# Kernel optimization log

Measured on AMD Instinct MI355X. Metric: run time of the kernel, lower is better.

The kernel has to match this reference:

```python
import jax, jax.numpy as jnp
import numpy as np

RADIUS = 0.4
NSAMPLE = 32
NORMALIZE_DP = True


def setup_inputs() -> dict:
    key = jax.random.key(0)
    k1, k2, k3 = jax.random.split(key, 3)
    B, N, K, C = 2, 16384, 4096, 128
    xyz = jax.random.normal(k1, (B, N, 3), dtype=jnp.float32)
    new_xyz = jax.random.normal(k2, (B, K, 3), dtype=jnp.float32)
    features = jax.random.normal(k3, (B, C, N), dtype=jnp.float32)
    return {"xyz": xyz, "new_xyz": new_xyz, "features": features}


def _ball_query(radius, nsample, xyz, new_xyz):
    # xyz: (B,N,3), new_xyz: (B,K,3) -> indices (B,K,nsample) int32
    N = xyz.shape[1]
    # squared distances via ||a||^2 + ||b||^2 - 2 a.b  -> (B,K,N)
    d2 = (jnp.sum(new_xyz * new_xyz, -1)[:, :, None]
          + jnp.sum(xyz * xyz, -1)[:, None, :]
          - 2.0 * jnp.einsum('bkd,bnd->bkn', new_xyz, xyz))
    mask = d2 < radius * radius
    # key = point index if inside ball else N (sentinel); take nsample smallest
    key = jnp.where(mask, jnp.arange(N, dtype=jnp.int32), jnp.int32(N))
    neg_top, _ = jax.lax.top_k(-key, nsample)  # (B,K,nsample)
    idx = -neg_top
    # pointnet2 semantics: pad with first in-radius index (0 if ball empty)
    first = idx[..., :1]
    first = jnp.where(first < N, first, 0)
    idx = jnp.where(idx < N, idx, first)
    return idx


def _group(features, idx):
    # features: (B,C,N), idx: (B,K,ns) -> (B,C,K,ns)
    return jax.vmap(lambda f, i: f[:, i])(features, idx)


def reference(xyz, new_xyz, features):
    idx = _ball_query(RADIUS, NSAMPLE, xyz, new_xyz)          # (B,K,ns)
    xyz_t = jnp.transpose(xyz, (0, 2, 1))                      # (B,3,N)
    grouped_xyz = _group(xyz_t, idx)                           # (B,3,K,ns)
    grouped_xyz = grouped_xyz - jnp.transpose(new_xyz, (0, 2, 1))[..., None]
    if NORMALIZE_DP:
        grouped_xyz = grouped_xyz / RADIUS
    grouped_features = _group(features, idx)                   # (B,C,K,ns)
    return (grouped_xyz, grouped_features)
```

## Files before the change

kernel.cpp:

```cpp
#include <hip/hip_runtime.h>

#define BB 2
#define NN 16384
#define KK 4096
#define CC 128
#define SS 32

typedef float vfloat4 __attribute__((ext_vector_type(4)));

__global__ __launch_bounds__(256) void transpose_prep_kernel(
    const float* __restrict__ feat, const float* __restrict__ xyz,
    float* __restrict__ feat_t, float* __restrict__ xyzw)
{
    __shared__ float tile[64][133];
    const int b  = blockIdx.x >> 8;
    const int n0 = (blockIdx.x & 255) * 64;
    const int t  = threadIdx.x;

    if (t < 64) {
        const int i = b * NN + n0 + t;
        const float* p = xyz + (size_t)i * 3;
        const float x = p[0], y = p[1], z = p[2];
        const float pp = __fadd_rn(__fadd_rn(__fmul_rn(x, x), __fmul_rn(y, y)),
                                   __fmul_rn(z, z));
        vfloat4 v = {x, y, z, pp};
        *(vfloat4*)(xyzw + (size_t)i * 4) = v;
    }

    const int ln = t & 63;
    const int cr = t >> 6;
#pragma unroll
    for (int p = 0; p < 32; ++p) {
        const int c = p * 4 + cr;
        tile[ln][c] = feat[((size_t)b * CC + c) * NN + n0 + ln];
    }
    __syncthreads();

    const int cl = t & 31;
    const int ns = t >> 5;
#pragma unroll
    for (int p = 0; p < 8; ++p) {
        const int n = ns + 8 * p;
        float* dst = feat_t + ((size_t)(b * NN + n0 + n)) * CC;
#pragma unroll
        for (int j = 0; j < 4; ++j)
            dst[cl + 32 * j] = tile[n][cl + 32 * j];
    }
}

__global__ __launch_bounds__(256) void ball_query_kernel(
    const float* __restrict__ xyzw,
    const float* __restrict__ new_xyz,
    int* __restrict__ idx_buf)
{
    __shared__ vfloat4 pts[256];

    const int t    = threadIdx.x;
    const int wave = t >> 6;
    const int lane = t & 63;
    const int qi   = blockIdx.x * 4 + wave;
    const int b    = qi >> 12;
    const int k    = qi & (KK - 1);

    const float R2 = (float)(0.4 * 0.4);

    const float* q = new_xyz + (size_t)(b * KK + k) * 3;
    const float qx = q[0], qy = q[1], qz = q[2];
    const float qq = __fadd_rn(__fadd_rn(__fmul_rn(qx, qx), __fmul_rn(qy, qy)),
                               __fmul_rn(qz, qz));

    const vfloat4* xw = (const vfloat4*)xyzw + (size_t)b * NN;
    int* out = idx_buf + (size_t)qi * SS;

    int cnt = 0;

    pts[t] = xw[t];
    __syncthreads();

    for (int base = 0; base < NN; base += 256) {
        const int nb = (base + 256 < NN) ? base + 256 : 0;
        const vfloat4 nxt = xw[nb + t];

        if (cnt < SS) {
            vfloat4 v0 = pts[lane];
            vfloat4 v1 = pts[64 + lane];
            vfloat4 v2 = pts[128 + lane];
            vfloat4 v3 = pts[192 + lane];

            auto d2test = [&](vfloat4 v) -> bool {
                const float dot = __fadd_rn(
                    __fadd_rn(__fmul_rn(qx, v.x), __fmul_rn(qy, v.y)),
                    __fmul_rn(qz, v.z));
                const float d2 = __fsub_rn(__fadd_rn(qq, v.w), __fmul_rn(2.0f, dot));
                return d2 < R2;
            };

            const bool i0 = d2test(v0);
            const bool i1 = d2test(v1);
            const bool i2 = d2test(v2);
            const bool i3 = d2test(v3);
            const unsigned long long m0 = __ballot(i0);
            const unsigned long long m1 = __ballot(i1);
            const unsigned long long m2 = __ballot(i2);
            const unsigned long long m3 = __ballot(i3);

            const int c0 = cnt;
            const int p0 = __popcll(m0), p1 = __popcll(m1);
            const int p2 = __popcll(m2), p3 = __popcll(m3);
            cnt = c0 + p0 + p1 + p2 + p3;

            if ((m0 | m1 | m2 | m3) != 0ull && c0 < SS) {
                const unsigned long long lt = (1ull << lane) - 1ull;
                int bs = c0;
                if (i0) { const int pos = bs + __popcll(m0 & lt);
                          if (pos < SS) out[pos] = base + lane; }
                bs += p0;
                if (i1) { const int pos = bs + __popcll(m1 & lt);
                          if (pos < SS) out[pos] = base + 64 + lane; }
                bs += p1;
                if (i2) { const int pos = bs + __popcll(m2 & lt);
                          if (pos < SS) out[pos] = base + 128 + lane; }
                bs += p2;
                if (i3) { const int pos = bs + __popcll(m3 & lt);
                          if (pos < SS) out[pos] = base + 192 + lane; }
            }
        }

        if (__syncthreads_and(cnt >= SS)) break;

        pts[t] = nxt;
        __syncthreads();
    }

    const int fill = (cnt > 0) ? out[0] : 0;
    if (lane < SS && lane >= cnt) out[lane] = fill;
}

__global__ __launch_bounds__(256) void group_kernel(
    const float* __restrict__ xyzw,
    const float* __restrict__ new_xyz,
    const float* __restrict__ feat_t,
    const int*   __restrict__ idx_buf,
    float* __restrict__ out)
{
    __shared__ float tile[SS * CC];
    __shared__ float txyz[3][SS];

    const int t    = threadIdx.x;
    const int l    = t & 63;
    const int w    = t >> 6;
    const int bk   = blockIdx.x;
    const int b    = bk >> 12;
    const int k    = bk & (KK - 1);
    const int half = l >> 5;
    const int cl   = l & 31;

#pragma unroll
    for (int p = 0; p < 4; ++p) {
        const int r = 8 * w + 2 * p;
        const int s = r + half;
        const int n = idx_buf[bk * SS + s];
        const int chunk = cl ^ ((s >> 2) & 7);
        const float* src = feat_t + ((size_t)(b * NN + n)) * CC + 4 * chunk;
        __builtin_amdgcn_global_load_lds(
            (const __attribute__((address_space(1))) void*)src,
            (__attribute__((address_space(3))) void*)(tile + r * CC),
            16, 0, 0);
    }

    if (t < SS) {
        const int n = idx_buf[bk * SS + t];
        const float* q = new_xyz + (size_t)bk * 3;
        const vfloat4 wv = *((const vfloat4*)xyzw + (size_t)b * NN + n);
        txyz[0][t] = (wv.x - q[0]) / 0.4f;
        txyz[1][t] = (wv.y - q[1]) / 0.4f;
        txyz[2][t] = (wv.z - q[2]) / 0.4f;
    }

    __syncthreads();

    float* out_xyz  = out;
    float* out_feat = out + (size_t)BB * 3 * KK * SS;

    const int sq = t & 7;
    const int c0 = t >> 3;
#pragma unroll
    for (int p = 0; p < 4; ++p) {
        const int c  = c0 + 32 * p;
        const int co = (((c >> 2) ^ sq) << 2) + (c & 3);
        vfloat4 v;
        v.x = tile[(4 * sq + 0) * CC + co];
        v.y = tile[(4 * sq + 1) * CC + co];
        v.z = tile[(4 * sq + 2) * CC + co];
        v.w = tile[(4 * sq + 3) * CC + co];
        __builtin_nontemporal_store(
            v, (vfloat4*)(out_feat + (((size_t)(b * CC + c) * KK + k) * SS + 4 * sq)));
    }

    if (t < 24) {
        const int d   = t >> 3;
        const int sq2 = t & 7;
        const vfloat4 v = *(vfloat4*)&txyz[d][4 * sq2];
        __builtin_nontemporal_store(
            v, (vfloat4*)(out_xyz + (((size_t)(b * 3 + d) * KK + k) * SS + 4 * sq2)));
    }
}

extern "C" void kernel_launch(void* const* d_in, const int* in_sizes, int n_in,
                              void* d_out, int out_size, void* d_ws, size_t ws_size,
                              hipStream_t stream) {
    const float* xyz     = (const float*)d_in[0];
    const float* new_xyz = (const float*)d_in[1];
    const float* feat    = (const float*)d_in[2];
    float* out = (float*)d_out;

    int*   idx_buf = (int*)d_ws;
    float* xyzw    = (float*)((char*)d_ws + (1 << 20));
    float* feat_t  = (float*)((char*)d_ws + (1 << 20) + (512 << 10));

    transpose_prep_kernel<<<dim3(BB * (NN / 64)), dim3(256), 0, stream>>>(
        feat, xyz, feat_t, xyzw);

    ball_query_kernel<<<dim3(BB * KK / 4), dim3(256), 0, stream>>>(
        xyzw, new_xyz, idx_buf);

    group_kernel<<<dim3(BB * KK), dim3(256), 0, stream>>>(
        xyzw, new_xyz, feat_t, idx_buf, out);
}
```

Measured before the change: 101.6 us.

## Sort queries by radial distance to balance ball-query early exit; vectorize transpose

Adds a single-block kernel that buckets query points by squared norm (per batch) and writes a permutation, so that each ball-query block handles four queries with similar distance from the origin and therefore similar early-exit points. This is meant to cut the time waves spend waiting on the slowest query in a block, and to order blocks by cost. The feature transpose now uses float4 global loads and stores instead of scalar ones. The costs are an extra serial single-block launch, scattered LDS atomics, and a qmap indirection.

```diff
diff --git a/kernel.cpp b/kernel.cpp
--- a/kernel.cpp
+++ b/kernel.cpp
@@ -5,6 +5,7 @@
 #define KK 4096
 #define CC 128
 #define SS 32
+#define BKK (BB * KK)
 
 typedef float vfloat4 __attribute__((ext_vector_type(4)));
 
@@ -27,30 +28,78 @@
         *(vfloat4*)(xyzw + (size_t)i * 4) = v;
     }
 
-    const int ln = t & 63;
-    const int cr = t >> 6;
-#pragma unroll
-    for (int p = 0; p < 32; ++p) {
-        const int c = p * 4 + cr;
-        tile[ln][c] = feat[((size_t)b * CC + c) * NN + n0 + ln];
-    }
-    __syncthreads();
-
-    const int cl = t & 31;
-    const int ns = t >> 5;
-#pragma unroll
-    for (int p = 0; p < 8; ++p) {
-        const int n = ns + 8 * p;
-        float* dst = feat_t + ((size_t)(b * NN + n0 + n)) * CC;
-#pragma unroll
-        for (int j = 0; j < 4; ++j)
-            dst[cl + 32 * j] = tile[n][cl + 32 * j];
+#pragma unroll
+    for (int i = 0; i < 8; ++i) {
+        const int li = i * 256 + t;
+        const int c  = li >> 4;
+        const int n4 = (li & 15) * 4;
+        const vfloat4 v = *(const vfloat4*)(feat + ((size_t)b * CC + c) * NN + n0 + n4);
+        tile[n4 + 0][c] = v.x;
+        tile[n4 + 1][c] = v.y;
+        tile[n4 + 2][c] = v.z;
+        tile[n4 + 3][c] = v.w;
+    }
+    __syncthreads();
+
+#pragma unroll
+    for (int i = 0; i < 8; ++i) {
+        const int li = i * 256 + t;
+        const int n  = li >> 5;
+        const int c4 = (li & 31) * 4;
+        vfloat4 v;
+        v.x = tile[n][c4 + 0];
+        v.y = tile[n][c4 + 1];
+        v.z = tile[n][c4 + 2];
+        v.w = tile[n][c4 + 3];
+        *(vfloat4*)(feat_t + ((size_t)(b * NN + n0 + n)) * CC + c4) = v;
+    }
+}
+
+__global__ __launch_bounds__(1024) void qsort_kernel(
+    const float* __restrict__ new_xyz,
+    int* __restrict__ qmap)
+{
+    __shared__ int hist[128];
+    __shared__ int base[128];
+    __shared__ unsigned char bk[BKK];
+
+    const int t = threadIdx.x;
+    if (t < 128) hist[t] = 0;
+    __syncthreads();
+
+#pragma unroll
+    for (int c = 0; c < BKK / 1024; ++c) {
+        const int q = c * 1024 + t;
+        const int b = q >> 12;
+        const float* p = new_xyz + (size_t)q * 3;
+        const float qq = p[0] * p[0] + p[1] * p[1] + p[2] * p[2];
+        int bkt = (int)(qq * 8.0f);
+        bkt = bkt > 63 ? 63 : bkt;
+        bkt |= (b << 6);
+        bk[q] = (unsigned char)bkt;
+        atomicAdd(&hist[bkt], 1);
+    }
+    __syncthreads();
+
+    if (t == 0) {
+        int s = 0;
+#pragma unroll
+        for (int i = 0; i < 128; ++i) { base[i] = s; s += hist[i]; }
+    }
+    __syncthreads();
+
+#pragma unroll
+    for (int c = 0; c < BKK / 1024; ++c) {
+        const int q = c * 1024 + t;
+        const int pos = atomicAdd(&base[bk[q]], 1);
+        qmap[pos] = q;
     }
 }
 
 __global__ __launch_bounds__(256) void ball_query_kernel(
     const float* __restrict__ xyzw,
     const float* __restrict__ new_xyz,
+    const int* __restrict__ qmap,
     int* __restrict__ idx_buf)
 {
     __shared__ vfloat4 pts[256];
@@ -58,7 +107,7 @@
     const int t    = threadIdx.x;
     const int wave = t >> 6;
     const int lane = t & 63;
-    const int qi   = blockIdx.x * 4 + wave;
+    const int qi   = qmap[blockIdx.x * 4 + wave];
     const int b    = qi >> 12;
     const int k    = qi & (KK - 1);
 
@@ -217,13 +266,16 @@
     int*   idx_buf = (int*)d_ws;
     float* xyzw    = (float*)((char*)d_ws + (1 << 20));
     float* feat_t  = (float*)((char*)d_ws + (1 << 20) + (512 << 10));
+    int*   qmap    = (int*)((char*)d_ws + (1 << 20) + (512 << 10) + (CC * NN * BB) * 4);
 
     transpose_prep_kernel<<<dim3(BB * (NN / 64)), dim3(256), 0, stream>>>(
         feat, xyz, feat_t, xyzw);
 
-    ball_query_kernel<<<dim3(BB * KK / 4), dim3(256), 0, stream>>>(
-        xyzw, new_xyz, idx_buf);
-
-    group_kernel<<<dim3(BB * KK), dim3(256), 0, stream>>>(
+    qsort_kernel<<<dim3(1), dim3(1024), 0, stream>>>(new_xyz, qmap);
+
+    ball_query_kernel<<<dim3(BKK / 4), dim3(256), 0, stream>>>(
+        xyzw, new_xyz, qmap, idx_buf);
+
+    group_kernel<<<dim3(BKK), dim3(256), 0, stream>>>(
         xyzw, new_xyz, feat_t, idx_buf, out);
 }
```

Result: no change. 99.91 us (-1.7%).
